# Performance work log

Measured on AMD Instinct MI355X. Metric: run time of the kernel, lower is better.

## Reference

```python
import jax, jax.numpy as jnp
import numpy as np

N = 100000
E = 1600000
F = 64
OUT = 7

def setup_inputs() -> dict:
    key = jax.random.key(0)
    k1, k2, k3, k4, k5 = jax.random.split(key, 5)
    x = jax.random.normal(k1, (N, F), dtype=jnp.float32)
    edge_index = jax.random.randint(k2, (2, E), 0, N, dtype=jnp.int64)
    W_l = jax.random.normal(k3, (F, OUT), dtype=jnp.float32) / np.sqrt(F)
    b_l = jax.random.normal(k4, (OUT,), dtype=jnp.float32) * 0.01
    W_r = jax.random.normal(k5, (F, OUT), dtype=jnp.float32) / np.sqrt(F)
    return {"x": x, "edge_index": edge_index, "W_l": W_l, "b_l": b_l, "W_r": W_r}

def reference(x, edge_index, W_l, b_l, W_r):
    # PyG SAGEConv (mean aggr): out = lin_l(mean_{j in N(i)} x_j) + lin_r(x_i), then relu
    src, dst = edge_index[0], edge_index[1]
    msgs = x[src]                                            # [E, F] gather
    agg = jax.ops.segment_sum(msgs, dst, num_segments=N)     # [N, F]
    cnt = jax.ops.segment_sum(jnp.ones((E,), dtype=x.dtype), dst, num_segments=N)
    mean = agg / jnp.maximum(cnt, 1.0)[:, None]              # isolated nodes -> 0
    out = mean @ W_l + b_l + x @ W_r                         # [N, 7]
    return jax.nn.relu(out)
```

## Files before the change

kernel.cpp:

```cpp
#include <hip/hip_runtime.h>

#define NN 100000
#define NE 1600000
#define FIN 64
#define FOUT 7

#define BSH 9
#define NBK 196
#define PBLK 2000
#define PTH  256
#define EPB  800
#define EPT  4
#define NCOPY 4
#define NCTR (NBK * NCOPY)
#define ROWS 200
#define SPLIT 4
#define RPS (PBLK / SPLIT)
#define ATH 512
#define SCAP 2560
#define PROJB 391
#define INVALID 0xFFFFFFFFu

__device__ __forceinline__ unsigned bf16r(float f) {
    unsigned u = __float_as_uint(f);
    return (u + 0x7fffu + ((u >> 16) & 1u)) >> 16;
}
__device__ __forceinline__ float bflo(unsigned u) { return __uint_as_float(u << 16); }
__device__ __forceinline__ float bfhi(unsigned u) { return __uint_as_float(u & 0xffff0000u); }

__global__ __launch_bounds__(256) void proj_kernel(
    const float* __restrict__ x, const float* __restrict__ Wl,
    const float* __restrict__ bl, const float* __restrict__ Wr,
    unsigned* __restrict__ z, float* __restrict__ outself, int n)
{
    int i = blockIdx.x * blockDim.x + threadIdx.x;
    if (i >= n) return;

    float al[FOUT], ar[FOUT];
#pragma unroll
    for (int j = 0; j < FOUT; ++j) { al[j] = 0.f; ar[j] = 0.f; }

    const float4* xr = (const float4*)(x + (size_t)i * FIN);
#pragma unroll
    for (int kk = 0; kk < FIN / 4; ++kk) {
        float4 xv = xr[kk];
        float v[4] = {xv.x, xv.y, xv.z, xv.w};
#pragma unroll
        for (int c = 0; c < 4; ++c) {
            int k = kk * 4 + c;
#pragma unroll
            for (int j = 0; j < FOUT; ++j) {
                al[j] = fmaf(v[c], Wl[k * FOUT + j], al[j]);
                ar[j] = fmaf(v[c], Wr[k * FOUT + j], ar[j]);
            }
        }
    }

    uint4 pk;
    pk.x = bf16r(al[0]) | (bf16r(al[1]) << 16);
    pk.y = bf16r(al[2]) | (bf16r(al[3]) << 16);
    pk.z = bf16r(al[4]) | (bf16r(al[5]) << 16);
    pk.w = bf16r(al[6]);
    ((uint4*)z)[i] = pk;

    float* o = outself + (size_t)i * FOUT;
#pragma unroll
    for (int j = 0; j < FOUT; ++j)
        o[j] = ar[j] + bl[j];
}

__global__ __launch_bounds__(PTH) void part_kernel(
    const int* __restrict__ eg, unsigned* __restrict__ part,
    unsigned short* __restrict__ offs)
{
    __shared__ unsigned st_cnt[NCTR];
    __shared__ unsigned st_start[NCTR];
    __shared__ unsigned stage[EPB];
    __shared__ unsigned wsum[NCOPY];

    const int t    = threadIdx.x;
    const int e0   = (int)blockIdx.x * EPB;
    const int lane = t & 63;
    const int wv   = t >> 6;

    for (int b = t; b < NCTR; b += PTH) st_cnt[b] = 0;
    __syncthreads();

    unsigned held[EPT], hcr[EPT];
#pragma unroll
    for (int j = 0; j < EPT; ++j) {
        int k = t + j * PTH;
        if (k < EPB) {
            unsigned s = (unsigned)eg[e0 + k];
            unsigned d = (unsigned)eg[NE + e0 + k];
            unsigned cidx = (d >> BSH) * NCOPY + wv;
            unsigned r = atomicAdd(&st_cnt[cidx], 1u);
            held[j] = ((d & 511u) << 17) | s;
            hcr[j]  = (cidx << 10) | r;
        } else hcr[j] = INVALID;
    }
    __syncthreads();

    {
        unsigned c[4], sum = 0;
#pragma unroll
        for (int q = 0; q < 4; ++q) {
            int idx = 4 * t + q;
            c[q] = (idx < NCTR) ? st_cnt[idx] : 0u;
            sum += c[q];
        }
        unsigned inc = sum;
#pragma unroll
        for (int off = 1; off < 64; off <<= 1) {
            unsigned v = (unsigned)__shfl_up((int)inc, off, 64);
            if (lane >= off) inc += v;
        }
        if (lane == 63) wsum[wv] = inc;
        __syncthreads();
        if (t == 0) {
            unsigned run = 0;
#pragma unroll
            for (int w = 0; w < NCOPY; ++w) { unsigned tmp = wsum[w]; wsum[w] = run; run += tmp; }
        }
        __syncthreads();
        unsigned base = wsum[wv] + inc - sum;
#pragma unroll
        for (int q = 0; q < 4; ++q) {
            int idx = 4 * t + q;
            if (idx < NCTR) st_start[idx] = base;
            base += c[q];
        }
    }
    __syncthreads();

#pragma unroll
    for (int j = 0; j < EPT; ++j) {
        if (hcr[j] != INVALID) {
            unsigned cidx = hcr[j] >> 10, r = hcr[j] & 0x3FFu;
            stage[st_start[cidx] + r] = held[j];
        }
    }

    if (t <= NBK)
        offs[(size_t)blockIdx.x * ROWS + t] =
            (unsigned short)((t == NBK) ? EPB : st_start[t * NCOPY]);
    __syncthreads();

    const uint4* sg = (const uint4*)stage;
    uint4* pg = (uint4*)(part + (size_t)blockIdx.x * EPB);
    for (int j = t; j < EPB / 4; j += PTH) pg[j] = sg[j];
}

__global__ __launch_bounds__(ATH) void acc_kernel(
    const unsigned short* __restrict__ offs, const unsigned* __restrict__ part,
    const unsigned* __restrict__ zb, float* __restrict__ partial)
{
    __shared__ unsigned s_cnt[512];
    __shared__ unsigned s_start[512];
    __shared__ unsigned s_pos[512];
    __shared__ unsigned sstage[SCAP];
    __shared__ unsigned wtot[8];

    const int t = threadIdx.x;
    const int k = blockIdx.x >> 2;
    const int s = blockIdx.x & 3;

    s_cnt[t] = 0;
    __syncthreads();

    unsigned rbase = 0, len = 0;
    if (t < RPS) {
        unsigned r = (unsigned)(s * RPS + t);
        unsigned o0 = offs[(size_t)r * ROWS + k];
        unsigned o1 = offs[(size_t)r * ROWS + k + 1];
        len   = o1 - o0;
        rbase = r * EPB + o0;
    }

    for (unsigned j = 0; j < len; ++j)
        atomicAdd(&s_cnt[part[rbase + j] >> 17], 1u);
    __syncthreads();

    unsigned cval = s_cnt[t], inc = cval;
#pragma unroll
    for (int off = 1; off < 64; off <<= 1) {
        unsigned v = (unsigned)__shfl_up((int)inc, off, 64);
        if ((t & 63) >= off) inc += v;
    }
    if ((t & 63) == 63) wtot[t >> 6] = inc;
    __syncthreads();
    if (t == 0) {
        unsigned run = 0;
#pragma unroll
        for (int w = 0; w < 8; ++w) { unsigned tmp = wtot[w]; wtot[w] = run; run += tmp; }
    }
    __syncthreads();
    {
        unsigned st = wtot[t >> 6] + inc - cval;
        s_start[t] = st;
        s_pos[t]   = st;
    }
    __syncthreads();

    for (unsigned j = 0; j < len; ++j) {
        unsigned e = part[rbase + j];
        unsigned p = atomicAdd(&s_pos[e >> 17], 1u);
        if (p < SCAP) sstage[p] = e & 0x1FFFFu;
    }
    __syncthreads();

    unsigned deg  = s_cnt[t];
    unsigned base = s_start[t];
    unsigned hi   = min(base + deg, (unsigned)SCAP);

    float a0 = 0.f, a1 = 0.f, a2 = 0.f, a3 = 0.f, a4 = 0.f, a5 = 0.f, a6 = 0.f;
    for (unsigned j = base; j < hi; ++j) {
        unsigned src = sstage[j];
        uint4 zr = ((const uint4*)zb)[src];
        a0 += bflo(zr.x); a1 += bfhi(zr.x);
        a2 += bflo(zr.y); a3 += bfhi(zr.y);
        a4 += bflo(zr.z); a5 += bfhi(zr.z);
        a6 += bflo(zr.w);
    }

    float* pp = partial + ((size_t)blockIdx.x * 512 + t) * 8;
    *(float4*)(pp)     = make_float4(a0, a1, a2, a3);
    *(float4*)(pp + 4) = make_float4(a4, a5, a6, (float)deg);
}

__global__ __launch_bounds__(256) void merge_kernel(
    const float* __restrict__ partial, float* __restrict__ out, int n)
{
    int i = blockIdx.x * blockDim.x + threadIdx.x;
    if (i >= n) return;
    int k = i >> BSH;
    int node = i & 511;

    float s0 = 0.f, s1 = 0.f, s2 = 0.f, s3 = 0.f, s4 = 0.f, s5 = 0.f, s6 = 0.f, cn = 0.f;
#pragma unroll
    for (int s = 0; s < SPLIT; ++s) {
        const float4* p = (const float4*)(partial + ((size_t)(k * SPLIT + s) * 512 + node) * 8);
        float4 a = p[0], b = p[1];
        s0 += a.x; s1 += a.y; s2 += a.z; s3 += a.w;
        s4 += b.x; s5 += b.y; s6 += b.z; cn += b.w;
    }
    float r = 1.0f / fmaxf(cn, 1.0f);
    float* o = out + (size_t)i * FOUT;
    o[0] = fmaxf(fmaf(s0, r, o[0]), 0.f);
    o[1] = fmaxf(fmaf(s1, r, o[1]), 0.f);
    o[2] = fmaxf(fmaf(s2, r, o[2]), 0.f);
    o[3] = fmaxf(fmaf(s3, r, o[3]), 0.f);
    o[4] = fmaxf(fmaf(s4, r, o[4]), 0.f);
    o[5] = fmaxf(fmaf(s5, r, o[5]), 0.f);
    o[6] = fmaxf(fmaf(s6, r, o[6]), 0.f);
}

extern "C" void kernel_launch(void* const* d_in, const int* in_sizes, int n_in,
                              void* d_out, int out_size, void* d_ws, size_t ws_size,
                              hipStream_t stream) {
    const float* x   = (const float*)d_in[0];
    const int*   edg = (const int*)d_in[1];
    const float* Wl  = (const float*)d_in[2];
    const float* bl  = (const float*)d_in[3];
    const float* Wr  = (const float*)d_in[4];
    float* out = (float*)d_out;

    unsigned*       z       = (unsigned*)d_ws;
    unsigned*       part    = z + (size_t)NN * 4;
    unsigned short* offs    = (unsigned short*)(part + (size_t)NE);
    float*          partial = (float*)(offs + (size_t)PBLK * ROWS);

    proj_kernel<<<PROJB, 256, 0, stream>>>(x, Wl, bl, Wr, z, out, NN);
    part_kernel<<<PBLK, PTH, 0, stream>>>(edg, part, offs);
    acc_kernel<<<NBK * SPLIT, ATH, 0, stream>>>(offs, part, z, partial);
    merge_kernel<<<(NN + 255) / 256, 256, 0, stream>>>(partial, out, NN);
}
```

Before: 131.0 us.

## Restructure accumulation: halve splits, keep edges in registers, split nodes across two threads

```diff
diff --git a/kernel.cpp b/kernel.cpp
--- a/kernel.cpp
+++ b/kernel.cpp
@@ -14,10 +14,12 @@
 #define NCOPY 4
 #define NCTR (NBK * NCOPY)
 #define ROWS 200
-#define SPLIT 4
+#define SPLIT 2
 #define RPS (PBLK / SPLIT)
-#define ATH 512
-#define SCAP 2560
+#define ATH 1024
+#define CAPR 8
+#define OVCAP 256
+#define SCAP 4608
 #define PROJB 391
 #define INVALID 0xFFFFFFFFu
 
@@ -157,15 +159,18 @@
 {
     __shared__ unsigned s_cnt[512];
     __shared__ unsigned s_start[512];
-    __shared__ unsigned s_pos[512];
     __shared__ unsigned sstage[SCAP];
+    __shared__ float    lacc[512 * 8];
+    __shared__ unsigned ovf[2 * OVCAP];
+    __shared__ unsigned novf;
     __shared__ unsigned wtot[8];
 
     const int t = threadIdx.x;
-    const int k = blockIdx.x >> 2;
-    const int s = blockIdx.x & 3;
-
-    s_cnt[t] = 0;
+    const int k = blockIdx.x >> 1;
+    const int s = blockIdx.x & 1;
+
+    if (t < 512) s_cnt[t] = 0;
+    if (t == 0) novf = 0;
     __syncthreads();
 
     unsigned rbase = 0, len = 0;
@@ -177,17 +182,40 @@
         rbase = r * EPB + o0;
     }
 
-    for (unsigned j = 0; j < len; ++j)
-        atomicAdd(&s_cnt[part[rbase + j] >> 17], 1u);
-    __syncthreads();
-
-    unsigned cval = s_cnt[t], inc = cval;
-#pragma unroll
-    for (int off = 1; off < 64; off <<= 1) {
-        unsigned v = (unsigned)__shfl_up((int)inc, off, 64);
-        if ((t & 63) >= off) inc += v;
-    }
-    if ((t & 63) == 63) wtot[t >> 6] = inc;
+    unsigned hsrc[CAPR], hnr[CAPR];
+#pragma unroll
+    for (int j = 0; j < CAPR; ++j) {
+        if (j < (int)len) {
+            unsigned e = part[rbase + j];
+            unsigned node = e >> 17;
+            unsigned r = atomicAdd(&s_cnt[node], 1u);
+            hsrc[j] = e & 0x1FFFFu;
+            hnr[j]  = (node << 16) | r;
+        } else hnr[j] = INVALID;
+    }
+    for (int j = CAPR; j < (int)len; ++j) {
+        unsigned e = part[rbase + j];
+        unsigned node = e >> 17;
+        unsigned r = atomicAdd(&s_cnt[node], 1u);
+        unsigned p = atomicAdd(&novf, 1u);
+        if (p < OVCAP) {
+            ovf[2 * p]     = (node << 16) | r;
+            ovf[2 * p + 1] = e & 0x1FFFFu;
+        }
+    }
+    __syncthreads();
+
+    unsigned cval = 0, inc = 0;
+    if (t < 512) {
+        cval = s_cnt[t];
+        inc = cval;
+#pragma unroll
+        for (int off = 1; off < 64; off <<= 1) {
+            unsigned v = (unsigned)__shfl_up((int)inc, off, 64);
+            if ((t & 63) >= off) inc += v;
+        }
+        if ((t & 63) == 63) wtot[t >> 6] = inc;
+    }
     __syncthreads();
     if (t == 0) {
         unsigned run = 0;
@@ -195,27 +223,34 @@
         for (int w = 0; w < 8; ++w) { unsigned tmp = wtot[w]; wtot[w] = run; run += tmp; }
     }
     __syncthreads();
-    {
-        unsigned st = wtot[t >> 6] + inc - cval;
-        s_start[t] = st;
-        s_pos[t]   = st;
-    }
-    __syncthreads();
-
-    for (unsigned j = 0; j < len; ++j) {
-        unsigned e = part[rbase + j];
-        unsigned p = atomicAdd(&s_pos[e >> 17], 1u);
-        if (p < SCAP) sstage[p] = e & 0x1FFFFu;
-    }
-    __syncthreads();
-
-    unsigned deg  = s_cnt[t];
-    unsigned base = s_start[t];
-    unsigned hi   = min(base + deg, (unsigned)SCAP);
+    if (t < 512) s_start[t] = wtot[t >> 6] + inc - cval;
+    __syncthreads();
+
+#pragma unroll
+    for (int j = 0; j < CAPR; ++j) {
+        if (hnr[j] != INVALID) {
+            unsigned node = hnr[j] >> 16, r = hnr[j] & 0xffffu;
+            unsigned p = s_start[node] + r;
+            if (p < SCAP) sstage[p] = hsrc[j];
+        }
+    }
+    for (unsigned q = t; q < min(novf, (unsigned)OVCAP); q += ATH) {
+        unsigned nr = ovf[2 * q], src = ovf[2 * q + 1];
+        unsigned p = s_start[nr >> 16] + (nr & 0xffffu);
+        if (p < SCAP) sstage[p] = src;
+    }
+    __syncthreads();
+
+    unsigned node = t & 511u;
+    unsigned half = (unsigned)t >> 9;
+    unsigned deg  = s_cnt[node];
+    unsigned base = s_start[node];
+    unsigned lo = half ? (deg >> 1) : 0u;
+    unsigned hi = half ? deg : (deg >> 1);
 
     float a0 = 0.f, a1 = 0.f, a2 = 0.f, a3 = 0.f, a4 = 0.f, a5 = 0.f, a6 = 0.f;
-    for (unsigned j = base; j < hi; ++j) {
-        unsigned src = sstage[j];
+    for (unsigned j = lo; j < hi && base + j < SCAP; ++j) {
+        unsigned src = sstage[base + j];
         uint4 zr = ((const uint4*)zb)[src];
         a0 += bflo(zr.x); a1 += bfhi(zr.x);
         a2 += bflo(zr.y); a3 += bfhi(zr.y);
@@ -223,9 +258,21 @@
         a6 += bflo(zr.w);
     }
 
-    float* pp = partial + ((size_t)blockIdx.x * 512 + t) * 8;
-    *(float4*)(pp)     = make_float4(a0, a1, a2, a3);
-    *(float4*)(pp + 4) = make_float4(a4, a5, a6, (float)deg);
+    if (half) {
+        float* L = &lacc[node * 8];
+        *(float4*)(L)     = make_float4(a0, a1, a2, a3);
+        *(float4*)(L + 4) = make_float4(a4, a5, a6, 0.f);
+    }
+    __syncthreads();
+
+    if (!half) {
+        const float* L = &lacc[node * 8];
+        a0 += L[0]; a1 += L[1]; a2 += L[2]; a3 += L[3];
+        a4 += L[4]; a5 += L[5]; a6 += L[6];
+        float* pp = partial + ((size_t)blockIdx.x * 512 + node) * 8;
+        *(float4*)(pp)     = make_float4(a0, a1, a2, a3);
+        *(float4*)(pp + 4) = make_float4(a4, a5, a6, (float)deg);
+    }
 }
 
 __global__ __launch_bounds__(256) void merge_kernel(
```

Measured after the change: 123.9 us. -5.5%, faster.

## Hold edge window in registers and unroll the first eight gathers per node

Applied to the files above, without the earlier changes.

```diff
diff --git a/kernel.cpp b/kernel.cpp
--- a/kernel.cpp
+++ b/kernel.cpp
@@ -15,9 +15,12 @@
 #define NCTR (NBK * NCOPY)
 #define ROWS 200
 #define SPLIT 4
+#define NTASK (NBK * SPLIT)
 #define RPS (PBLK / SPLIT)
 #define ATH 512
-#define SCAP 2560
+#define WSLOT 12
+#define OVCAP 256
+#define SCAP 3968
 #define PROJB 391
 #define INVALID 0xFFFFFFFFu
 
@@ -157,37 +160,72 @@
 {
     __shared__ unsigned s_cnt[512];
     __shared__ unsigned s_start[512];
-    __shared__ unsigned s_pos[512];
-    __shared__ unsigned sstage[SCAP];
+    __shared__ __align__(16) unsigned sstage[SCAP + 8];
+    __shared__ unsigned ovf[2 * OVCAP];
+    __shared__ unsigned novf;
     __shared__ unsigned wtot[8];
 
-    const int t = threadIdx.x;
-    const int k = blockIdx.x >> 2;
-    const int s = blockIdx.x & 3;
+    const int t    = threadIdx.x;
+    const int lane = t & 63;
+    const int k    = blockIdx.x >> 2;
+    const int sp   = blockIdx.x & 3;
 
     s_cnt[t] = 0;
+    if (t == 0) novf = 0;
     __syncthreads();
 
     unsigned rbase = 0, len = 0;
     if (t < RPS) {
-        unsigned r = (unsigned)(s * RPS + t);
+        unsigned r = (unsigned)(sp * RPS + t);
         unsigned o0 = offs[(size_t)r * ROWS + k];
         unsigned o1 = offs[(size_t)r * ROWS + k + 1];
         len   = o1 - o0;
         rbase = r * EPB + o0;
     }
 
-    for (unsigned j = 0; j < len; ++j)
-        atomicAdd(&s_cnt[part[rbase + j] >> 17], 1u);
-    __syncthreads();
-
-    unsigned cval = s_cnt[t], inc = cval;
+    unsigned sh = rbase & 3u;
+    const uint4* p4 = (const uint4*)part;
+    unsigned wbase = rbase >> 2;
+    uint4 W0 = len ? p4[wbase]     : make_uint4(0, 0, 0, 0);
+    uint4 W1 = len ? p4[wbase + 1] : make_uint4(0, 0, 0, 0);
+    uint4 W2 = len ? p4[wbase + 2] : make_uint4(0, 0, 0, 0);
+    unsigned win[WSLOT] = {W0.x, W0.y, W0.z, W0.w,
+                           W1.x, W1.y, W1.z, W1.w,
+                           W2.x, W2.y, W2.z, W2.w};
+    unsigned hsrc[WSLOT], hnr[WSLOT];
+    unsigned F = min(len, WSLOT - sh);
+#pragma unroll
+    for (int q = 0; q < WSLOT; ++q) {
+        unsigned uq = (unsigned)q;
+        if (uq >= sh && uq < sh + F) {
+            unsigned e = win[q];
+            unsigned node = e >> 17;
+            unsigned rk = atomicAdd(&s_cnt[node], 1u);
+            hsrc[q] = e & 0x1FFFFu;
+            hnr[q]  = (node << 16) | rk;
+        } else hnr[q] = INVALID;
+    }
+    for (unsigned j = F; j < len; ++j) {
+        unsigned e = part[rbase + j];
+        unsigned node = e >> 17;
+        unsigned rk = atomicAdd(&s_cnt[node], 1u);
+        unsigned pp = atomicAdd(&novf, 1u);
+        if (pp < OVCAP) {
+            ovf[2 * pp]     = (node << 16) | rk;
+            ovf[2 * pp + 1] = e & 0x1FFFFu;
+        }
+    }
+    __syncthreads();
+
+    unsigned cval = s_cnt[t];
+    unsigned pcnt = (cval + 3u) & ~3u;
+    unsigned inc = pcnt;
 #pragma unroll
     for (int off = 1; off < 64; off <<= 1) {
         unsigned v = (unsigned)__shfl_up((int)inc, off, 64);
-        if ((t & 63) >= off) inc += v;
-    }
-    if ((t & 63) == 63) wtot[t >> 6] = inc;
+        if (lane >= off) inc += v;
+    }
+    if (lane == 63) wtot[t >> 6] = inc;
     __syncthreads();
     if (t == 0) {
         unsigned run = 0;
@@ -195,28 +233,45 @@
         for (int w = 0; w < 8; ++w) { unsigned tmp = wtot[w]; wtot[w] = run; run += tmp; }
     }
     __syncthreads();
-    {
-        unsigned st = wtot[t >> 6] + inc - cval;
-        s_start[t] = st;
-        s_pos[t]   = st;
-    }
-    __syncthreads();
-
-    for (unsigned j = 0; j < len; ++j) {
-        unsigned e = part[rbase + j];
-        unsigned p = atomicAdd(&s_pos[e >> 17], 1u);
-        if (p < SCAP) sstage[p] = e & 0x1FFFFu;
-    }
-    __syncthreads();
-
-    unsigned deg  = s_cnt[t];
-    unsigned base = s_start[t];
-    unsigned hi   = min(base + deg, (unsigned)SCAP);
+    unsigned mybase = wtot[t >> 6] + inc - pcnt;
+    s_start[t] = mybase;
+    __syncthreads();
+
+#pragma unroll
+    for (int q = 0; q < WSLOT; ++q) {
+        if (hnr[q] != INVALID) {
+            unsigned node = hnr[q] >> 16, rk = hnr[q] & 0xffffu;
+            unsigned pp = s_start[node] + rk;
+            if (pp < SCAP) sstage[pp] = hsrc[q];
+        }
+    }
+    for (unsigned q = t; q < min(novf, (unsigned)OVCAP); q += ATH) {
+        unsigned nr = ovf[2 * q], src = ovf[2 * q + 1];
+        unsigned pp = s_start[nr >> 16] + (nr & 0xffffu);
+        if (pp < SCAP) sstage[pp] = src;
+    }
+    __syncthreads();
+
+    unsigned deg = s_cnt[t];
+    uint4 C0 = *(const uint4*)&sstage[mybase];
+    uint4 C1 = *(const uint4*)&sstage[mybase + 4];
+    unsigned sv[8] = {C0.x, C0.y, C0.z, C0.w, C1.x, C1.y, C1.z, C1.w};
 
     float a0 = 0.f, a1 = 0.f, a2 = 0.f, a3 = 0.f, a4 = 0.f, a5 = 0.f, a6 = 0.f;
-    for (unsigned j = base; j < hi; ++j) {
-        unsigned src = sstage[j];
+#pragma unroll
+    for (int j = 0; j < 8; ++j) {
+        unsigned src = ((unsigned)j < deg) ? sv[j] : 0u;
+        float m = ((unsigned)j < deg) ? 1.0f : 0.0f;
         uint4 zr = ((const uint4*)zb)[src];
+        a0 = fmaf(m, bflo(zr.x), a0); a1 = fmaf(m, bfhi(zr.x), a1);
+        a2 = fmaf(m, bflo(zr.y), a2); a3 = fmaf(m, bfhi(zr.y), a3);
+        a4 = fmaf(m, bflo(zr.z), a4); a5 = fmaf(m, bfhi(zr.z), a5);
+        a6 = fmaf(m, bflo(zr.w), a6);
+    }
+    for (unsigned j = 8; j < deg; ++j) {
+        unsigned pp = mybase + j;
+        if (pp >= SCAP) break;
+        uint4 zr = ((const uint4*)zb)[sstage[pp]];
         a0 += bflo(zr.x); a1 += bfhi(zr.x);
         a2 += bflo(zr.y); a3 += bfhi(zr.y);
         a4 += bflo(zr.z); a5 += bfhi(zr.z);
@@ -267,11 +322,11 @@
 
     unsigned*       z       = (unsigned*)d_ws;
     unsigned*       part    = z + (size_t)NN * 4;
-    unsigned short* offs    = (unsigned short*)(part + (size_t)NE);
+    unsigned short* offs    = (unsigned short*)(part + (size_t)NE + 16);
     float*          partial = (float*)(offs + (size_t)PBLK * ROWS);
 
     proj_kernel<<<PROJB, 256, 0, stream>>>(x, Wl, bl, Wr, z, out, NN);
     part_kernel<<<PBLK, PTH, 0, stream>>>(edg, part, offs);
-    acc_kernel<<<NBK * SPLIT, ATH, 0, stream>>>(offs, part, z, partial);
+    acc_kernel<<<NTASK, ATH, 0, stream>>>(offs, part, z, partial);
     merge_kernel<<<(NN + 255) / 256, 256, 0, stream>>>(partial, out, NN);
 }
```

New measurement: 123.4 us. 5.8% less time.
